# Performance work log

Measured on AMD Instinct MI355X. Metric: run time of the kernel, lower is better.

Reference implementation:

```python
import jax, jax.numpy as jnp
import numpy as np

H = 16
DH = 64
THETA = 10000.0


def setup_inputs() -> dict:
    key = jax.random.key(0)
    ks = jax.random.split(key, 9)
    B, M, R = 4, 1024, 256
    d = H * DH
    s = 0.05
    return {
        "Pq": jax.random.normal(ks[0], (B, M, R), jnp.float32) * s,
        "Pk": jax.random.normal(ks[1], (B, M, R), jnp.float32) * s,
        "Pv": jax.random.normal(ks[2], (B, M, R), jnp.float32) * s,
        "Vq": jax.random.normal(ks[3], (R, d), jnp.float32) * s,
        "Vk": jax.random.normal(ks[4], (R, d), jnp.float32) * s,
        "Vv": jax.random.normal(ks[5], (R, d), jnp.float32) * s,
        "bq": jax.random.normal(ks[6], (d,), jnp.float32) * s,
        "bk": jax.random.normal(ks[7], (d,), jnp.float32) * s,
        "bv": jax.random.normal(ks[8], (d,), jnp.float32) * s,
        "attention_mask": jnp.ones((B, M), jnp.int32),
        "position_ids": jnp.tile(jnp.arange(M, dtype=jnp.int32), (B, 1)),
    }


def _rope_cos_sin(position_ids):
    # half-dim frequencies, matching the kernel's half-half rotation
    half = DH // 2
    inv_freq = 1.0 / (THETA ** (jnp.arange(0, half, dtype=jnp.float32) / half))
    ang = position_ids.astype(jnp.float32)[..., None] * inv_freq  # [B,M,half]
    return jnp.cos(ang), jnp.sin(ang)


def _rotate(x, cos, sin):
    # x: [B,H,M,dh]; cos/sin: [B,M,half] -> broadcast over heads
    half = DH // 2
    x0, x1 = x[..., :half], x[..., half:]
    c = cos[:, None, :, :]
    s = sin[:, None, :, :]
    return jnp.concatenate([x0 * c - x1 * s, x0 * s + x1 * c], axis=-1)


def reference(Pq, Pk, Pv, Vq, Vk, Vv, bq, bk, bv, attention_mask, position_ids):
    B, M, R = Pq.shape
    # reconstruct per-head Q/K/V from low-rank factors
    Vq3 = Vq.reshape(R, H, DH)
    Vk3 = Vk.reshape(R, H, DH)
    Vv3 = Vv.reshape(R, H, DH)
    q = jnp.einsum("bmr,rhd->bhmd", Pq, Vq3) + bq.reshape(H, DH)[None, :, None, :]
    k = jnp.einsum("bmr,rhd->bhmd", Pk, Vk3) + bk.reshape(H, DH)[None, :, None, :]
    v = jnp.einsum("bmr,rhd->bhmd", Pv, Vv3) + bv.reshape(H, DH)[None, :, None, :]
    cos, sin = _rope_cos_sin(position_ids)
    q = _rotate(q, cos, sin)
    k = _rotate(k, cos, sin)
    scale = 1.0 / jnp.sqrt(jnp.float32(DH))
    scores = jnp.einsum("bhmd,bhnd->bhmn", q, k) * scale  # [B,H,M,M]
    valid = attention_mask.astype(bool)
    pad = valid[:, None, :, None] & valid[:, None, None, :]
    scores = jnp.where(pad, scores, -jnp.inf)
    p = jax.nn.softmax(scores, axis=-1)
    out = jnp.einsum("bhmn,bhnd->bhmd", p, v)
    return out
```

## Files before the change

kernel.cpp:

```cpp
#include <hip/hip_runtime.h>
#include <hip/hip_bf16.h>
#include <math.h>

#define BB 4
#define MM 1024
#define RR 256
#define HH 16
#define DHH 64
#define DD (HH*DHH)

typedef __attribute__((ext_vector_type(8))) short short8;
typedef __attribute__((ext_vector_type(4))) float f32x4;

static __device__ __forceinline__ unsigned short f2bf(float x) {
    __hip_bfloat16 h = __float2bfloat16(x);
    return *(unsigned short*)&h;
}

#if defined(__has_builtin)
#  if __has_builtin(__builtin_amdgcn_exp2f)
#    define EXP2F(x) __builtin_amdgcn_exp2f(x)
#  endif
#endif
#ifndef EXP2F
#  define EXP2F(x) __expf((x) * 0.6931471805599453f)
#endif

static __device__ __forceinline__ unsigned pack_bf16_rh(float a, float b) {
    unsigned ua = __builtin_bit_cast(unsigned, a) + 0x8000u;
    unsigned ub = __builtin_bit_cast(unsigned, b) + 0x8000u;
    return __builtin_amdgcn_perm(ub, ua, 0x07060302u);
}

static __device__ __forceinline__ void gload_lds16(const void* g, void* l) {
    __builtin_amdgcn_global_load_lds(
        (const __attribute__((address_space(1))) unsigned int*)g,
        (__attribute__((address_space(3))) unsigned int*)l, 16, 0, 0);
}

__global__ __launch_bounds__(256) void prep_kernel(
    const float* __restrict__ Pq, const float* __restrict__ Pk, const float* __restrict__ Pv,
    const float* __restrict__ Vq, const float* __restrict__ Vk, const float* __restrict__ Vv,
    __hip_bfloat16* __restrict__ VTq, __hip_bfloat16* __restrict__ VTk,
    __hip_bfloat16* __restrict__ VTv, __hip_bfloat16* __restrict__ Pb)
{
    const int t = threadIdx.x;
    if (blockIdx.x < 768) {
        const int z   = blockIdx.x / 256;
        const int rem = blockIdx.x % 256;
        const int r0  = (rem & 7) * 32;
        const int d0  = (rem >> 3) * 32;
        const float* V = (z == 0) ? Vq : (z == 1) ? Vk : Vv;
        __hip_bfloat16* VT = (z == 0) ? VTq : (z == 1) ? VTk : VTv;

        __shared__ __hip_bfloat16 Ts[32][33];
        {
            const int row = t >> 3;
            const int c4  = (t & 7) * 4;
            float4 f = *(const float4*)&V[(size_t)(r0 + row) * DD + d0 + c4];
            Ts[row][c4 + 0] = __float2bfloat16(f.x);
            Ts[row][c4 + 1] = __float2bfloat16(f.y);
            Ts[row][c4 + 2] = __float2bfloat16(f.z);
            Ts[row][c4 + 3] = __float2bfloat16(f.w);
        }
        __syncthreads();
        {
            const int orow = t >> 3;
            const int oc4  = (t & 7) * 4;
            union { unsigned short u[4]; uint2 v; } pk;
            #pragma unroll
            for (int i = 0; i < 4; ++i) pk.u[i] = *(unsigned short*)&Ts[oc4 + i][orow];
            *(uint2*)&VT[(size_t)(d0 + orow) * RR + r0 + oc4] = pk.v;
        }
    } else {
        const size_t n4 = (size_t)BB * MM * RR / 4;
        size_t i = (size_t)(blockIdx.x - 768) * 256 + t;
        const int which = (int)(i / n4);
        const size_t off = i - (size_t)which * n4;
        const float* P = (which == 0) ? Pq : (which == 1) ? Pk : Pv;
        float4 f = *(const float4*)(P + off * 4);
        union { unsigned short u[4]; uint2 v; } pk;
        pk.u[0] = f2bf(f.x); pk.u[1] = f2bf(f.y); pk.u[2] = f2bf(f.z); pk.u[3] = f2bf(f.w);
        *(uint2*)((unsigned short*)Pb + (size_t)which * BB * MM * RR + off * 4) = pk.v;
    }
}

__global__ __launch_bounds__(256) void svd_gemm(
    const __hip_bfloat16* __restrict__ Pb,
    const __hip_bfloat16* __restrict__ VTq, const __hip_bfloat16* __restrict__ VTk,
    const __hip_bfloat16* __restrict__ VTv,
    const float* __restrict__ bq, const float* __restrict__ bk, const float* __restrict__ bv,
    const int* __restrict__ pos_ids,
    __hip_bfloat16* __restrict__ qout, __hip_bfloat16* __restrict__ kout,
    __hip_bfloat16* __restrict__ vTout)
{
    const int which = blockIdx.z;
    const short* P = (const short*)Pb + (size_t)which * BB * MM * RR;
    const __hip_bfloat16* VT = (which == 0) ? VTq : (which == 1) ? VTk : VTv;
    const float* bias        = (which == 0) ? bq : (which == 1) ? bk : bv;

    const int h   = blockIdx.y;
    const int bm0 = blockIdx.x * 256;
    const int b   = bm0 >> 10;
    const int m0  = bm0 & 1023;
    const int tid = threadIdx.x;
    const int lane = tid & 63;
    const int w    = tid >> 6;
    const int l15  = lane & 15;
    const int quad = lane >> 4;

    __shared__ alignas(16) short SM[256 * 72 + 64 * 72];
    short* As = SM;
    short* Bs = SM + 256 * 72;

    f32x4 acc[4][4];
    #pragma unroll
    for (int mt = 0; mt < 4; ++mt)
        #pragma unroll
        for (int dt = 0; dt < 4; ++dt) acc[mt][dt] = (f32x4){0.f, 0.f, 0.f, 0.f};

    for (int kc = 0; kc < 4; ++kc) {
        #pragma unroll
        for (int i = 0; i < 8; ++i) {
            int u = tid + i * 256;
            int row = u >> 3;
            int cg  = (u & 7) * 8;
            *(uint4*)&As[row * 72 + cg] =
                *(const uint4*)&P[(size_t)(bm0 + row) * RR + kc * 64 + cg];
        }
        #pragma unroll
        for (int i = 0; i < 2; ++i) {
            int u = tid + i * 256;
            int row = u >> 3;
            int cg  = (u & 7) * 8;
            *(uint4*)&Bs[row * 72 + cg] =
                *(const uint4*)((const short*)VT + (size_t)(h * 64 + row) * RR + kc * 64 + cg);
        }
        __syncthreads();

        #pragma unroll
        for (int ks = 0; ks < 2; ++ks) {
            short8 a[4];
            #pragma unroll
            for (int mt = 0; mt < 4; ++mt)
                a[mt] = *(const short8*)&As[(w * 64 + mt * 16 + l15) * 72 + ks * 32 + quad * 8];
            #pragma unroll
            for (int dt = 0; dt < 4; ++dt) {
                short8 bf = *(const short8*)&Bs[(dt * 16 + l15) * 72 + ks * 32 + quad * 8];
                #pragma unroll
                for (int mt = 0; mt < 4; ++mt)
                    acc[mt][dt] = __builtin_amdgcn_mfma_f32_16x16x32_bf16(a[mt], bf, acc[mt][dt], 0, 0, 0);
            }
        }
        __syncthreads();
    }

    #pragma unroll
    for (int dt = 0; dt < 4; ++dt) {
        float bc = bias[h * 64 + dt * 16 + l15];
        #pragma unroll
        for (int mt = 0; mt < 4; ++mt)
            #pragma unroll
            for (int r = 0; r < 4; ++r) acc[mt][dt][r] += bc;
    }

    if (which < 2) {
        __hip_bfloat16* out = (which == 0) ? qout : kout;
        int pm[4][4];
        #pragma unroll
        for (int mt = 0; mt < 4; ++mt)
            #pragma unroll
            for (int r = 0; r < 4; ++r)
                pm[mt][r] = pos_ids[bm0 + w * 64 + mt * 16 + quad * 4 + r];
        float cB[2][4][4], sB[2][4][4];
        #pragma unroll
        for (int f2 = 0; f2 < 2; ++f2) {
            float invf = __powf(10000.0f, -(float)(f2 * 16 + l15) * (1.0f / 32.0f));
            #pragma unroll
            for (int mt = 0; mt < 4; ++mt)
                #pragma unroll
                for (int r = 0; r < 4; ++r) {
                    float ang = (float)pm[mt][r] * invf;
                    __sincosf(ang, &sB[f2][mt][r], &cB[f2][mt][r]);
                }
        }
        #pragma unroll
        for (int dt = 0; dt < 4; ++dt) {
            const int cd = dt * 16 + l15;
            const int f2 = dt & 1;
            #pragma unroll
            for (int mt = 0; mt < 4; ++mt)
                #pragma unroll
                for (int r = 0; r < 4; ++r) {
                    float x  = acc[mt][dt][r];
                    float xp = acc[mt][dt ^ 2][r];
                    float c = cB[f2][mt][r], s = sB[f2][mt][r];
                    float val = (dt < 2) ? (x * c - xp * s) : (xp * s + x * c);
                    int m = m0 + w * 64 + mt * 16 + quad * 4 + r;
                    out[(((size_t)b * HH + h) * MM + m) * DHH + cd] = __float2bfloat16(val);
                }
        }
    } else {
        short* Tt = SM;
        __syncthreads();
        #pragma unroll
        for (int dt = 0; dt < 4; ++dt)
            #pragma unroll
            for (int mt = 0; mt < 4; ++mt) {
                union { unsigned short u[4]; uint2 v; } pk;
                #pragma unroll
                for (int r = 0; r < 4; ++r) pk.u[r] = f2bf(acc[mt][dt][r]);
                *(uint2*)&Tt[(dt * 16 + l15) * 264 + w * 64 + mt * 16 + quad * 4] = pk.v;
            }
        __syncthreads();
        #pragma unroll
        for (int it = 0; it < 8; ++it) {
            int u = tid + it * 256;
            int row = u >> 5;
            int seg = u & 31;
            *(uint4*)&vTout[(((size_t)b * HH + h) * DHH + row) * MM + m0 + seg * 8] =
                *(const uint4*)&Tt[row * 264 + seg * 8];
        }
    }
}

__global__ __launch_bounds__(256, 2) void attn_kernel(
    const __hip_bfloat16* __restrict__ q, const __hip_bfloat16* __restrict__ k,
    const __hip_bfloat16* __restrict__ vT,
    const int* __restrict__ mask, float* __restrict__ out)
{
    const int bh   = blockIdx.x & 63;
    const int qt   = blockIdx.x >> 6;
    const int b    = bh >> 4;
    const int tid  = threadIdx.x;
    const int lane = tid & 63;
    const int w    = tid >> 6;
    const int l15  = lane & 15;
    const int quad = lane >> 4;
    const int q0   = qt * 128;

    __shared__ alignas(16) short KtL[2][128 * 64];
    __shared__ alignas(16) __hip_bfloat16 Vt[2][64][136];

    const short* kbase = (const short*)k  + (size_t)bh * MM * DHH;
    const short* vbase = (const short*)vT + (size_t)bh * DHH * MM;

    short8 qa[2][2];
    #pragma unroll
    for (int mt = 0; mt < 2; ++mt) {
        const short* qb = (const short*)q +
            ((size_t)bh * MM + q0 + w * 32 + mt * 16 + l15) * DHH + quad * 8;
        qa[mt][0] = *(const short8*)(qb);
        qa[mt][1] = *(const short8*)(qb + 32);
    }

    short8 onesB;
    #pragma unroll
    for (int i = 0; i < 8; ++i) onesB[i] = (short)0x3F80;

    f32x4 Ot[2][4];
    f32x4 Lacc[2];
    #pragma unroll
    for (int mt = 0; mt < 2; ++mt) {
        #pragma unroll
        for (int dt = 0; dt < 4; ++dt) Ot[mt][dt] = (f32x4){0.f, 0.f, 0.f, 0.f};
        Lacc[mt] = (f32x4){0.f, 0.f, 0.f, 0.f};
    }

    const int* maskb = mask + b * MM;
    const float k2 = 0.125f * 1.44269504089f;

    const int p0 = quad ^ (l15 & 7);
    const int p1 = (quad + 4) ^ (l15 & 7);

    {
        #pragma unroll
        for (int pass = 0; pass < 4; ++pass) {
            int u = tid + pass * 256;
            int row = u >> 3;
            int gl  = (u & 7) ^ (row & 7);
            gload_lds16(kbase + (size_t)row * DHH + gl * 8, &KtL[0][u * 8]);
        }
        #pragma unroll
        for (int pass = 0; pass < 4; ++pass) {
            int u = tid + pass * 256;
            int row = u >> 4, c = u & 15;
            union { uint4 q4; uint2 h2[2]; } vld;
            vld.q4 = *(const uint4*)(vbase + (size_t)row * MM + c * 8);
            int g = c >> 3, c6 = c & 7;
            int base0 = g * 64 + (c6 >> 2) * 32 + (c6 & 1) * 16 + ((c6 >> 1) & 1) * 4;
            *(uint2*)&Vt[0][row][base0]     = vld.h2[0];
            *(uint2*)&Vt[0][row][base0 + 8] = vld.h2[1];
        }
        __syncthreads();
    }

    for (int nc = 0; nc < MM / 128; ++nc) {
        const int cur = nc & 1;
        const int n0  = nc * 128;

        uint4 vreg[4];
        if (nc < 7) {
            const short* vb2 = vbase + n0 + 128;
            #pragma unroll
            for (int pass = 0; pass < 4; ++pass) {
                int u = tid + pass * 256, row = u >> 4, c = u & 15;
                vreg[pass] = *(const uint4*)(vb2 + (size_t)row * MM + c * 8);
            }
            const short* kb2 = kbase + (size_t)(n0 + 128) * DHH;
            #pragma unroll
            for (int pass = 0; pass < 4; ++pass) {
                int u = tid + pass * 256;
                int row = u >> 3;
                int gl  = (u & 7) ^ (row & 7);
                gload_lds16(kb2 + (size_t)row * DHH + gl * 8, &KtL[cur ^ 1][u * 8]);
            }
        }

        unsigned long long bal0 = __ballot(maskb[n0 + lane] != 0);
        unsigned long long bal1 = __ballot(maskb[n0 + 64 + lane] != 0);

        f32x4 S[2][8];
        __builtin_amdgcn_s_setprio(1);
        #pragma unroll
        for (int t = 0; t < 8; ++t) {
            const short* krow = &KtL[cur][(t * 16 + l15) * 64];
            short8 ka0 = *(const short8*)(krow + p0 * 8);
            short8 ka1 = *(const short8*)(krow + p1 * 8);
            #pragma unroll
            for (int mt = 0; mt < 2; ++mt) {
                f32x4 c = (f32x4){0.f, 0.f, 0.f, 0.f};
                c = __builtin_amdgcn_mfma_f32_16x16x32_bf16(ka0, qa[mt][0], c, 0, 0, 0);
                c = __builtin_amdgcn_mfma_f32_16x16x32_bf16(ka1, qa[mt][1], c, 0, 0, 0);
                S[mt][t] = c;
            }
        }
        __builtin_amdgcn_s_setprio(0);

        if ((bal0 & bal1) == ~0ull) {
            #pragma unroll
            for (int t = 0; t < 8; ++t)
                #pragma unroll
                for (int r = 0; r < 4; ++r)
                    #pragma unroll
                    for (int mt = 0; mt < 2; ++mt)
                        S[mt][t][r] = EXP2F(S[mt][t][r] * k2);
        } else {
            #pragma unroll
            for (int t = 0; t < 8; ++t) {
                unsigned bits = (unsigned)((t < 4 ? bal0 : bal1) >> ((t & 3) * 16 + quad * 4));
                #pragma unroll
                for (int r = 0; r < 4; ++r) {
                    float sb = ((bits >> r) & 1u) ? 0.0f : -1e30f;
                    #pragma unroll
                    for (int mt = 0; mt < 2; ++mt)
                        S[mt][t][r] = EXP2F(fmaf(S[mt][t][r], k2, sb));
                }
            }
        }

        short8 pa[2][4];
        #pragma unroll
        for (int mt = 0; mt < 2; ++mt)
            #pragma unroll
            for (int p = 0; p < 4; ++p) {
                union { unsigned u[4]; short8 s; } pk;
                pk.u[0] = pack_bf16_rh(S[mt][2*p][0],   S[mt][2*p][1]);
                pk.u[1] = pack_bf16_rh(S[mt][2*p][2],   S[mt][2*p][3]);
                pk.u[2] = pack_bf16_rh(S[mt][2*p+1][0], S[mt][2*p+1][1]);
                pk.u[3] = pack_bf16_rh(S[mt][2*p+1][2], S[mt][2*p+1][3]);
                pa[mt][p] = pk.s;
            }

        __builtin_amdgcn_s_setprio(1);
        #pragma unroll
        for (int p = 0; p < 4; ++p) {
            #pragma unroll
            for (int dt = 0; dt < 4; ++dt) {
                short8 vb = *(const short8*)&Vt[cur][dt * 16 + l15][p * 32 + quad * 8];
                #pragma unroll
                for (int mt = 0; mt < 2; ++mt)
                    Ot[mt][dt] = __builtin_amdgcn_mfma_f32_16x16x32_bf16(pa[mt][p], vb, Ot[mt][dt], 0, 0, 0);
            }
            #pragma unroll
            for (int mt = 0; mt < 2; ++mt)
                Lacc[mt] = __builtin_amdgcn_mfma_f32_16x16x32_bf16(pa[mt][p], onesB, Lacc[mt], 0, 0, 0);
        }
        __builtin_amdgcn_s_setprio(0);

        if (nc < 7) {
            #pragma unroll
            for (int pass = 0; pass < 4; ++pass) {
                int u = tid + pass * 256, row = u >> 4, c = u & 15;
                union { uint4 q4; uint2 h2[2]; } vld;
                vld.q4 = vreg[pass];
                int g = c >> 3, c6 = c & 7;
                int base0 = g * 64 + (c6 >> 2) * 32 + (c6 & 1) * 16 + ((c6 >> 1) & 1) * 4;
                *(uint2*)&Vt[cur ^ 1][row][base0]     = vld.h2[0];
                *(uint2*)&Vt[cur ^ 1][row][base0 + 8] = vld.h2[1];
            }
        }
        __syncthreads();
    }

    #pragma unroll
    for (int mt = 0; mt < 2; ++mt) {
        float* ob = out + ((size_t)bh * MM + q0 + w * 32 + mt * 16) * DHH;
        #pragma unroll
        for (int r = 0; r < 4; ++r) {
            float ir = 1.0f / Lacc[mt][r];
            #pragma unroll
            for (int dt = 0; dt < 4; ++dt)
                ob[(quad * 4 + r) * DHH + dt * 16 + l15] = Ot[mt][dt][r] * ir;
        }
    }
}

extern "C" void kernel_launch(void* const* d_in, const int* in_sizes, int n_in,
                              void* d_out, int out_size, void* d_ws, size_t ws_size,
                              hipStream_t stream) {
    const float* Pq = (const float*)d_in[0];
    const float* Pk = (const float*)d_in[1];
    const float* Pv = (const float*)d_in[2];
    const float* Vq = (const float*)d_in[3];
    const float* Vk = (const float*)d_in[4];
    const float* Vv = (const float*)d_in[5];
    const float* bq = (const float*)d_in[6];
    const float* bk = (const float*)d_in[7];
    const float* bv = (const float*)d_in[8];
    const int* mask = (const int*)d_in[9];
    const int* pos  = (const int*)d_in[10];
    float* out = (float*)d_out;

    const size_t qkv_elems = (size_t)BB * HH * MM * DHH;
    __hip_bfloat16* qb  = (__hip_bfloat16*)d_ws;
    __hip_bfloat16* kb  = qb + qkv_elems;
    __hip_bfloat16* vT  = kb + qkv_elems;
    __hip_bfloat16* VTq = vT + qkv_elems;
    __hip_bfloat16* VTk = VTq + (size_t)DD * RR;
    __hip_bfloat16* VTv = VTk + (size_t)DD * RR;
    __hip_bfloat16* Pb  = VTv + (size_t)DD * RR;

    prep_kernel<<<768 + 3 * BB * MM * RR / 4 / 256, 256, 0, stream>>>(
        Pq, Pk, Pv, Vq, Vk, Vv, VTq, VTk, VTv, Pb);

    dim3 gG(BB * MM / 256, HH, 3);
    svd_gemm<<<gG, 256, 0, stream>>>(Pb, VTq, VTk, VTv, bq, bk, bv, pos, qb, kb, vT);

    attn_kernel<<<BB * HH * (MM / 128), 256, 0, stream>>>(qb, kb, vT, mask, out);
}
```

Measured before the change: 129.1 us.

## Load V operands straight from global into registers, dropping the LDS V buffer

Removes the shared-memory V tile and its transposing stores. Each lane now loads its V MFMA operands directly from global memory into register double buffers (vA/vB), prefetched one chunk ahead and split in two halves around the PV MFMAs. The main loop is unrolled by two so the register buffers swap statically. This trades LDS traffic and writes for many small 8-byte global loads and a large increase in register use, which may lower occupancy under launch_bounds(256,2).

After: 207.8 us. 60.9% more time.

```diff
diff --git a/kernel.cpp b/kernel.cpp
--- a/kernel.cpp
+++ b/kernel.cpp
@@ -240,10 +240,10 @@
     const int q0   = qt * 128;
 
     __shared__ alignas(16) short KtL[2][128 * 64];
-    __shared__ alignas(16) __hip_bfloat16 Vt[2][64][136];
 
     const short* kbase = (const short*)k  + (size_t)bh * MM * DHH;
     const short* vbase = (const short*)vT + (size_t)bh * DHH * MM;
+    const short* vrow  = vbase + (size_t)l15 * MM + quad * 4;
 
     short8 qa[2][2];
     #pragma unroll
@@ -273,6 +273,21 @@
     const int p0 = quad ^ (l15 & 7);
     const int p1 = (quad + 4) ^ (l15 & 7);
 
+    short8 vA[4][4], vB[4][4];
+
+    auto vload2 = [&](short8 (&v)[4][4], int pbase, int n0) {
+        #pragma unroll
+        for (int p = 0; p < 2; ++p)
+            #pragma unroll
+            for (int dt = 0; dt < 4; ++dt) {
+                const short* a = vrow + (size_t)dt * 16 * MM + n0 + (pbase + p) * 32;
+                union { uint2 h2[2]; short8 s; } u;
+                u.h2[0] = *(const uint2*)(a);
+                u.h2[1] = *(const uint2*)(a + 16);
+                v[pbase + p][dt] = u.s;
+            }
+    };
+
     {
         #pragma unroll
         for (int pass = 0; pass < 4; ++pass) {
@@ -281,39 +296,23 @@
             int gl  = (u & 7) ^ (row & 7);
             gload_lds16(kbase + (size_t)row * DHH + gl * 8, &KtL[0][u * 8]);
         }
-        #pragma unroll
-        for (int pass = 0; pass < 4; ++pass) {
-            int u = tid + pass * 256;
-            int row = u >> 4, c = u & 15;
-            union { uint4 q4; uint2 h2[2]; } vld;
-            vld.q4 = *(const uint4*)(vbase + (size_t)row * MM + c * 8);
-            int g = c >> 3, c6 = c & 7;
-            int base0 = g * 64 + (c6 >> 2) * 32 + (c6 & 1) * 16 + ((c6 >> 1) & 1) * 4;
-            *(uint2*)&Vt[0][row][base0]     = vld.h2[0];
-            *(uint2*)&Vt[0][row][base0 + 8] = vld.h2[1];
-        }
-        __syncthreads();
-    }
-
-    for (int nc = 0; nc < MM / 128; ++nc) {
-        const int cur = nc & 1;
-        const int n0  = nc * 128;
-
-        uint4 vreg[4];
-        if (nc < 7) {
-            const short* vb2 = vbase + n0 + 128;
-            #pragma unroll
-            for (int pass = 0; pass < 4; ++pass) {
-                int u = tid + pass * 256, row = u >> 4, c = u & 15;
-                vreg[pass] = *(const uint4*)(vb2 + (size_t)row * MM + c * 8);
-            }
+        vload2(vA, 0, 0);
+        vload2(vA, 2, 0);
+        __syncthreads();
+    }
+
+    auto chunk = [&](int n0, const short* Kr, short* Kw,
+                     short8 (&vc)[4][4], short8 (&vn)[4][4]) {
+        const bool pf = (n0 + 128) < MM;
+        if (pf) {
+            vload2(vn, 0, n0 + 128);
             const short* kb2 = kbase + (size_t)(n0 + 128) * DHH;
             #pragma unroll
             for (int pass = 0; pass < 4; ++pass) {
                 int u = tid + pass * 256;
                 int row = u >> 3;
                 int gl  = (u & 7) ^ (row & 7);
-                gload_lds16(kb2 + (size_t)row * DHH + gl * 8, &KtL[cur ^ 1][u * 8]);
+                gload_lds16(kb2 + (size_t)row * DHH + gl * 8, Kw + (size_t)u * 8);
             }
         }
 
@@ -324,7 +323,7 @@
         __builtin_amdgcn_s_setprio(1);
         #pragma unroll
         for (int t = 0; t < 8; ++t) {
-            const short* krow = &KtL[cur][(t * 16 + l15) * 64];
+            const short* krow = Kr + (size_t)(t * 16 + l15) * 64;
             short8 ka0 = *(const short8*)(krow + p0 * 8);
             short8 ka1 = *(const short8*)(krow + p1 * 8);
             #pragma unroll
@@ -374,33 +373,41 @@
 
         __builtin_amdgcn_s_setprio(1);
         #pragma unroll
-        for (int p = 0; p < 4; ++p) {
-            #pragma unroll
-            for (int dt = 0; dt < 4; ++dt) {
-                short8 vb = *(const short8*)&Vt[cur][dt * 16 + l15][p * 32 + quad * 8];
+        for (int p = 0; p < 2; ++p) {
+            #pragma unroll
+            for (int dt = 0; dt < 4; ++dt)
                 #pragma unroll
                 for (int mt = 0; mt < 2; ++mt)
-                    Ot[mt][dt] = __builtin_amdgcn_mfma_f32_16x16x32_bf16(pa[mt][p], vb, Ot[mt][dt], 0, 0, 0);
-            }
+                    Ot[mt][dt] = __builtin_amdgcn_mfma_f32_16x16x32_bf16(pa[mt][p], vc[p][dt], Ot[mt][dt], 0, 0, 0);
             #pragma unroll
             for (int mt = 0; mt < 2; ++mt)
                 Lacc[mt] = __builtin_amdgcn_mfma_f32_16x16x32_bf16(pa[mt][p], onesB, Lacc[mt], 0, 0, 0);
         }
         __builtin_amdgcn_s_setprio(0);
 
-        if (nc < 7) {
-            #pragma unroll
-            for (int pass = 0; pass < 4; ++pass) {
-                int u = tid + pass * 256, row = u >> 4, c = u & 15;
-                union { uint4 q4; uint2 h2[2]; } vld;
-                vld.q4 = vreg[pass];
-                int g = c >> 3, c6 = c & 7;
-                int base0 = g * 64 + (c6 >> 2) * 32 + (c6 & 1) * 16 + ((c6 >> 1) & 1) * 4;
-                *(uint2*)&Vt[cur ^ 1][row][base0]     = vld.h2[0];
-                *(uint2*)&Vt[cur ^ 1][row][base0 + 8] = vld.h2[1];
-            }
-        }
-        __syncthreads();
+        if (pf) vload2(vn, 2, n0 + 128);
+
+        __builtin_amdgcn_s_setprio(1);
+        #pragma unroll
+        for (int p = 2; p < 4; ++p) {
+            #pragma unroll
+            for (int dt = 0; dt < 4; ++dt)
+                #pragma unroll
+                for (int mt = 0; mt < 2; ++mt)
+                    Ot[mt][dt] = __builtin_amdgcn_mfma_f32_16x16x32_bf16(pa[mt][p], vc[p][dt], Ot[mt][dt], 0, 0, 0);
+            #pragma unroll
+            for (int mt = 0; mt < 2; ++mt)
+                Lacc[mt] = __builtin_amdgcn_mfma_f32_16x16x32_bf16(pa[mt][p], onesB, Lacc[mt], 0, 0, 0);
+        }
+        __builtin_amdgcn_s_setprio(0);
+
+        __syncthreads();
+    };
+
+    #pragma unroll 1
+    for (int it = 0; it < 4; ++it) {
+        chunk(it * 256,       KtL[0], KtL[1], vA, vB);
+        chunk(it * 256 + 128, KtL[1], KtL[0], vB, vA);
     }
 
     #pragma unroll
```
